# Optimization experiments

Measured on AMD Instinct MI355X. Metric: run time of the kernel, lower is better.

The kernel has to match this reference:

```python
import jax, jax.numpy as jnp
import numpy as np

HEADS = 16
EPS = 1e-5

def _ln(t):
    # LayerNorm over last axis, no affine params
    mu = jnp.mean(t, axis=-1, keepdims=True)
    var = jnp.var(t, axis=-1, keepdims=True)
    return (t - mu) / jnp.sqrt(var + EPS)

def setup_inputs() -> dict:
    key = jax.random.key(0)
    ks = jax.random.split(key, 8)
    b, n, dim, mlp_dim = 4, 2048, 1024, 4096
    s = lambda d: 1.0 / np.sqrt(d)
    return {
        "x": jax.random.normal(ks[0], (b, n, dim), dtype=jnp.float32),
        "Wqkv": jax.random.uniform(ks[1], (dim, 3 * dim), jnp.float32, -s(dim), s(dim)),
        "W1": jax.random.uniform(ks[2], (dim, mlp_dim), jnp.float32, -s(dim), s(dim)),
        "b1": jax.random.uniform(ks[3], (mlp_dim,), jnp.float32, -s(dim), s(dim)),
        "W2": jax.random.uniform(ks[4], (mlp_dim, dim), jnp.float32, -s(mlp_dim), s(mlp_dim)),
        "b2": jax.random.uniform(ks[5], (dim,), jnp.float32, -s(mlp_dim), s(mlp_dim)),
        "Wout": jax.random.uniform(ks[6], (dim, dim), jnp.float32, -s(dim), s(dim)),
        "bout": jax.random.uniform(ks[7], (dim,), jnp.float32, -s(dim), s(dim)),
    }

def reference(x, Wqkv, W1, b1, W2, b2, Wout, bout):
    b, n, dim = x.shape
    h = HEADS
    d = dim // h
    scale = dim ** (-0.5)  # NOTE: module scales by full dim, not head_dim
    qkv = x @ Wqkv  # [b, n, 3*dim]
    qkv = qkv.reshape(b, n, 3, h, d).transpose(2, 0, 3, 1, 4)  # [3, b, h, n, d]
    q, k, v = qkv[0], qkv[1], qkv[2]
    q, k = _ln(q), _ln(k)
    dots = jnp.einsum('bhid,bhjd->bhij', q, k) * scale
    attn = jax.nn.softmax(dots, axis=-1)
    attn_v = jnp.einsum('bhij,bhjd->bhid', attn, v)
    attn_v = attn_v.transpose(0, 2, 1, 3).reshape(b, n, dim)
    attn_out = attn_v @ Wout + bout
    parallel = jax.nn.gelu(x @ W1 + b1, approximate=False) @ W2 + b2
    return _ln(attn_out + parallel)
```

## Files before the change

### kernel.cpp

```cpp
#include <hip/hip_runtime.h>

typedef __attribute__((ext_vector_type(8))) short s16x8;
typedef __attribute__((ext_vector_type(4))) short s16x4;
typedef __attribute__((ext_vector_type(4))) float f32x4;
typedef __attribute__((ext_vector_type(16))) float f32x16;
typedef __attribute__((ext_vector_type(2))) unsigned uint2v;

#define DEVINL __device__ __forceinline__

DEVINL float b2f(short u){ return __uint_as_float(((unsigned)(unsigned short)u) << 16); }
DEVINL short f2bf(float f){
  unsigned u = __float_as_uint(f);
  u += 0x7fffu + ((u >> 16) & 1u);
  return (short)(u >> 16);
}
DEVINL unsigned cvtpk(float lo, float hi){
  unsigned r;
  asm("v_cvt_pk_bf16_f32 %0, %1, %2" : "=v"(r) : "v"(lo), "v"(hi));
  return r;
}
DEVINL float max3f(float a, float b, float c){
  float r; asm("v_max3_f32 %0, %1, %2, %3" : "=v"(r) : "v"(a), "v"(b), "v"(c)); return r;
}

#if __has_builtin(__builtin_amdgcn_exp2f)
#define EXP2F __builtin_amdgcn_exp2f
#else
#define EXP2F exp2f
#endif

DEVINL f32x4 mfma32(s16x8 a, s16x8 b, f32x4 c){
  return __builtin_amdgcn_mfma_f32_16x16x32_bf16(a, b, c, 0, 0, 0);
}
DEVINL f32x16 mfma3216(s16x8 a, s16x8 b, f32x16 c){
  return __builtin_amdgcn_mfma_f32_32x32x16_bf16(a, b, c, 0, 0, 0);
}

DEVINL uint2v pl32swap(unsigned a, unsigned b){
#if __has_builtin(__builtin_amdgcn_permlane32_swap)
  return __builtin_amdgcn_permlane32_swap(a, b, false, false);
#else
  asm volatile("v_permlane32_swap_b32 %0, %1" : "+v"(a), "+v"(b));
  uint2v r; r[0] = a; r[1] = b; return r;
#endif
}

typedef const unsigned __attribute__((address_space(1)))* gas1;
typedef unsigned __attribute__((address_space(3)))* las3;
DEVINL void gload16(const short* g, short* l){
  __builtin_amdgcn_global_load_lds((gas1)g, (las3)l, 16, 0, 0);
}

#define CFENCE asm volatile("" ::: "memory")
#define PBAR  do{ CFENCE; __builtin_amdgcn_sched_barrier(0); __builtin_amdgcn_s_barrier(); \
                  __builtin_amdgcn_sched_barrier(0); CFENCE; }while(0)
#define VMW8 asm volatile("s_waitcnt vmcnt(8)" ::: "memory")
#define VMW4 asm volatile("s_waitcnt vmcnt(4)" ::: "memory")
#define VMW0 asm volatile("s_waitcnt vmcnt(0)" ::: "memory")
#define PRIO1 __builtin_amdgcn_s_setprio(1)
#define PRIO0 __builtin_amdgcn_s_setprio(0)

static const int Bc   = 4;
static const int Nc   = 2048;
static const int DIM  = 1024;
static const int Tc   = Bc * Nc;
static const int MLP  = 4096;
static const int D3   = 3072;

static const size_t OFF_XB    = 0;
static const size_t OFF_WQKVT = OFF_XB    + 16777216;
static const size_t OFF_W1T   = OFF_WQKVT + 6291456;
static const size_t OFF_W2T   = OFF_W1T   + 8388608;
static const size_t OFF_WOUTT = OFF_W2T   + 8388608;
static const size_t OFF_QKV   = OFF_WOUTT + 2097152;
static const size_t OFF_QLN   = OFF_QKV   + 50331648;
static const size_t OFF_KLN   = OFF_QLN   + 16777216;
static const size_t OFF_VT    = OFF_KLN   + 16777216;
static const size_t OFF_ATTNV = OFF_VT    + 16777216;
static const size_t OFF_H     = OFF_QKV;
static const size_t OFF_S2    = OFF_KLN;

__global__ __launch_bounds__(256) void conv_x(const float* __restrict__ x, short* __restrict__ xb){
  size_t i = ((size_t)blockIdx.x * 256 + threadIdx.x) * 8;
  f32x4 v0 = *(const f32x4*)(x + i);
  f32x4 v1 = *(const f32x4*)(x + i + 4);
  s16x8 o;
#pragma unroll
  for (int j = 0; j < 4; ++j){ o[j] = f2bf(v0[j]); o[4+j] = f2bf(v1[j]); }
  *(s16x8*)(xb + i) = o;
}

__global__ __launch_bounds__(256) void transpose_conv(const float* __restrict__ W, short* __restrict__ Wt,
                                                      int K, int N){
  __shared__ float tile[32][33];
  int ntx = N >> 5;
  int tx = blockIdx.x % ntx, ty = blockIdx.x / ntx;
  int r = threadIdx.x >> 3, c = (threadIdx.x & 7) * 4;
  f32x4 v = *(const f32x4*)(W + (size_t)(ty*32 + r)*N + tx*32 + c);
  tile[r][c] = v[0]; tile[r][c+1] = v[1]; tile[r][c+2] = v[2]; tile[r][c+3] = v[3];
  __syncthreads();
  s16x4 o;
#pragma unroll
  for (int j = 0; j < 4; ++j) o[j] = f2bf(tile[c+j][r]);
  *(s16x4*)(Wt + (size_t)(tx*32 + r)*K + ty*32 + c) = o;
}

template<int ACT, int FUSED>
__global__ __launch_bounds__(256, 2) void gemmCF(const short* __restrict__ A, const short* __restrict__ A2,
                                                 const short* __restrict__ Bt, const short* __restrict__ Bt2,
                                                 short* __restrict__ C,
                                                 const float* __restrict__ bias, const float* __restrict__ bias2,
                                                 int M, int N, int K1, int K2){
  __shared__ short lds[32768];

  const int tid = threadIdx.x;
  const int w = tid >> 6, lane = tid & 63;
  const int lr = lane & 15, g = lane >> 4;
  const int wr = w >> 1, wc = w & 1;
  const int NT1 = K1 >> 6;
  const int NT = NT1 + (FUSED ? (K2 >> 6) : 0);
  const int NIT = NT >> 1;

  const int nbn = N >> 7;
  const int cpx = gridDim.x >> 3;
  const int bid = (int)blockIdx.x;
  const int sw = (bid & 7)*cpx + (bid >> 3);
  const int nbn8 = nbn >> 3;
  const int T8 = sw >> 6, t64 = sw & 63;
  const int bm = (T8 / nbn8)*8 + (t64 >> 3);
  const int bn = (T8 % nbn8)*8 + (t64 & 7);

  const int l2 = lane >> 2;
  const int gsw = ((lane & 3) - ((lane >> 3) & 3)) & 3;
  const int cof = gsw * 8;
  const int qsw8 = ((g + (lr >> 1)) & 3) * 8;

  const short* ap0h = A  + (size_t)(bm*128 + w*16 + l2)*K1 + cof;
  const short* bp0h = Bt + (size_t)(bn*128 + w*16 + l2)*K1 + cof;
  const short* ap0a = FUSED ? (A2  + (size_t)(bm*128 + w*16 + l2)*K2 + cof) : nullptr;
  const short* bp0a = FUSED ? (Bt2 + (size_t)(bn*128 + w*16 + l2)*K2 + cof) : nullptr;

  auto stA = [&](int s, int T_, int kk){
    short* d0 = lds + s*4096 + w*512;
    if (FUSED && T_ >= NT1){
      size_t off = (size_t)(T_ - NT1)*64 + kk*32;
      gload16(ap0a + off, d0);
      gload16(ap0a + (size_t)64*K2 + off, d0 + 2048);
    } else {
      size_t off = (size_t)T_*64 + kk*32;
      gload16(ap0h + off, d0);
      gload16(ap0h + (size_t)64*K1 + off, d0 + 2048);
    }
  };
  auto stB = [&](int s, int T_, int kk){
    short* d0 = lds + 16384 + s*4096 + w*512;
    if (FUSED && T_ >= NT1){
      size_t off = (size_t)(T_ - NT1)*64 + kk*32;
      gload16(bp0a + off, d0);
      gload16(bp0a + (size_t)64*K2 + off, d0 + 2048);
    } else {
      size_t off = (size_t)T_*64 + kk*32;
      gload16(bp0h + off, d0);
      gload16(bp0h + (size_t)64*K1 + off, d0 + 2048);
    }
  };

#define LDA(s, mi) (*(const s16x8*)&lds[(s)*4096 + (wr*64 + (mi)*16 + lr)*32 + qsw8])
#define LDB(s, ni) (*(const s16x8*)&lds[16384 + (s)*4096 + (wc*64 + (ni)*16 + lr)*32 + qsw8])

  f32x4 acc[4][4] = {};
#define MM(ai, r) \
  acc[r][0]=mfma32(ai,b0,acc[r][0]); acc[r][1]=mfma32(ai,b1,acc[r][1]); \
  acc[r][2]=mfma32(ai,b2,acc[r][2]); acc[r][3]=mfma32(ai,b3,acc[r][3]);
#define RD(s) s16x8 a0=LDA(s,0),a1=LDA(s,1),a2=LDA(s,2),a3=LDA(s,3), \
                    b0=LDB(s,0),b1=LDB(s,1),b2=LDB(s,2),b3=LDB(s,3);
#define MM16 MM(a0,0) MM(a1,1) MM(a2,2) MM(a3,3)

  stA(0,0,0); stB(0,0,0);
  stA(1,0,1); stB(1,0,1);
  stA(2,1,0); stB(2,1,0);
  VMW8;
  PBAR;

  for (int i = 0; i < NIT; ++i){
    const int t = i << 1;
    const bool more = (i + 1 < NIT);
    {
      RD(0)
      stA(3, t+1, 1); stB(3, t+1, 1);
      PBAR; PRIO1; MM16 PRIO0;
      VMW8;
      PBAR;
    }
    {
      RD(1)
      if (more){ stA(0, t+2, 0); stB(0, t+2, 0); }
      PBAR; PRIO1; MM16 PRIO0;
      if (more){ VMW8; } else { VMW4; }
      PBAR;
    }
    {
      RD(2)
      if (more){ stA(1, t+2, 1); stB(1, t+2, 1); }
      PBAR; PRIO1; MM16 PRIO0;
      if (more){ VMW8; } else { VMW0; }
      PBAR;
    }
    {
      RD(3)
      if (more){ stA(2, t+3, 0); stB(2, t+3, 0); }
      PBAR; PRIO1; MM16 PRIO0;
      if (more){ VMW8; }
      PBAR;
    }
  }
#undef MM
#undef RD
#undef MM16
#undef LDA
#undef LDB

#pragma unroll
  for (int a = 0; a < 4; ++a){
#pragma unroll
    for (int ni = 0; ni < 4; ++ni){
      const int col = wc*64 + ni*16 + lr;
      float bv = bias ? bias[bn*128 + col] : 0.f;
      if (FUSED && bias2) bv += bias2[bn*128 + col];
      f32x4 v = acc[a][ni];
#pragma unroll
      for (int ii = 0; ii < 4; ++ii){
        float val = v[ii] + bv;
        if constexpr (ACT) val = 0.5f*val*(1.f + erff(val*0.70710678118f));
        lds[(wr*64 + a*16 + 4*g + ii)*128 + col] = f2bf(val);
      }
    }
  }
  __syncthreads();
  const size_t crow0 = (size_t)bm * 128;
  const int ch = (tid & 15) * 8;
#pragma unroll
  for (int p = 0; p < 8; ++p){
    const int row = p*16 + (tid >> 4);
    *(s16x8*)&C[(crow0 + row)*N + bn*128 + ch] = *(const s16x8*)&lds[row*128 + ch];
  }
}

__global__ __launch_bounds__(256) void ln_reorg(const short* __restrict__ qkv, short* __restrict__ qln,
                                                short* __restrict__ kln, short* __restrict__ vtb){
  __shared__ short vtile[64*72];
  int bh = blockIdx.x >> 5, tch = blockIdx.x & 31;
  int b = bh >> 4, h = bh & 15;
  int tq = threadIdx.x >> 2, j = threadIdx.x & 3;
  size_t row = (size_t)b*Nc + tch*64 + tq;
  const short* base = qkv + row*D3 + h*64 + j*16;
  size_t orow = ((size_t)bh*Nc + tch*64 + tq)*64 + j*16;

#pragma unroll
  for (int part = 0; part < 2; ++part){
    const short* src = base + part*DIM;
    s16x8 u0 = *(const s16x8*)src;
    s16x8 u1 = *(const s16x8*)(src + 8);
    float f[16]; float s = 0.f, sq = 0.f;
#pragma unroll
    for (int i = 0; i < 8; ++i){ f[i] = b2f(u0[i]); f[8+i] = b2f(u1[i]); }
#pragma unroll
    for (int i = 0; i < 16; ++i){ s += f[i]; sq += f[i]*f[i]; }
    s  += __shfl_xor(s, 1);  s  += __shfl_xor(s, 2);
    sq += __shfl_xor(sq, 1); sq += __shfl_xor(sq, 2);
    float mu = s * (1.f/64.f);
    float var = sq * (1.f/64.f) - mu*mu;
    float inv = rsqrtf(var + 1e-5f) * (part == 0 ? 0.04508422003f : 1.f);
    s16x8 o0, o1;
#pragma unroll
    for (int i = 0; i < 8; ++i){ o0[i] = f2bf((f[i]-mu)*inv); o1[i] = f2bf((f[8+i]-mu)*inv); }
    short* dst = (part == 0 ? qln : kln) + orow;
    *(s16x8*)dst = o0; *(s16x8*)(dst + 8) = o1;
  }

  s16x8 v0 = *(const s16x8*)(base + 2*DIM);
  s16x8 v1 = *(const s16x8*)(base + 2*DIM + 8);
  *(s16x8*)&vtile[tq*72 + j*16]     = v0;
  *(s16x8*)&vtile[tq*72 + j*16 + 8] = v1;
  __syncthreads();
  s16x8 o0, o1;
#pragma unroll
  for (int i = 0; i < 8; ++i){
    o0[i] = vtile[(j*16 + i)*72 + tq];
    o1[i] = vtile[(j*16 + 8 + i)*72 + tq];
  }
  short* vdst = vtb + ((size_t)bh*64 + tq)*Nc + tch*64 + j*16;
  *(s16x8*)vdst = o0; *(s16x8*)(vdst + 8) = o1;
}

__global__ __launch_bounds__(256) void attn_kern(const short* __restrict__ qln, const short* __restrict__ kln,
                                                 const short* __restrict__ vtb, short* __restrict__ attnv){
  __shared__ short Ks[2][64*72];
  __shared__ short Vs[2][64*72];
  const int tid = threadIdx.x;
  const int bh = blockIdx.x >> 4, qt = blockIdx.x & 15;
  const int b = bh >> 4, h = bh & 15;
  const int w = tid >> 6, lane = tid & 63;
  const int lq = lane & 31, hi = lane >> 5;
  const int qrow = qt*128 + w*32 + lq;

  const short* qp = qln + ((size_t)bh*Nc + qrow)*64 + hi*8;
  s16x8 qf[4];
#pragma unroll
  for (int m = 0; m < 4; ++m) qf[m] = *(const s16x8*)(qp + m*16);

  f32x16 o0 = {0,0,0,0,0,0,0,0,0,0,0,0,0,0,0,0};
  f32x16 o1 = {0,0,0,0,0,0,0,0,0,0,0,0,0,0,0,0};
  float mrun = -INFINITY, l = 0.f;

  const int sr = tid >> 3;
  const int sc = (tid & 7) * 8;
  const short* kb0 = kln + (size_t)bh*Nc*64;
  const short* vb0 = vtb + (size_t)bh*64*Nc;

  s16x8 kr0, kr1, vr0, vr1;
  {
    kr0 = *(const s16x8*)(kb0 + (size_t)sr*64 + sc);
    kr1 = *(const s16x8*)(kb0 + (size_t)(32 + sr)*64 + sc);
    vr0 = *(const s16x8*)(vb0 + (size_t)sr*Nc + sc);
    vr1 = *(const s16x8*)(vb0 + (size_t)(32 + sr)*Nc + sc);
  }

  for (int kt = 0; kt < 32; ++kt){
    const int cur = kt & 1;
    *(s16x8*)&Ks[cur][sr*72 + sc]        = kr0;
    *(s16x8*)&Ks[cur][(32 + sr)*72 + sc] = kr1;
    *(s16x8*)&Vs[cur][sr*72 + sc]        = vr0;
    *(s16x8*)&Vs[cur][(32 + sr)*72 + sc] = vr1;
    __syncthreads();
    if (kt + 1 < 32){
      const short* kb = kb0 + (size_t)(kt+1)*64*64;
      const short* vb = vb0 + (kt+1)*64;
      kr0 = *(const s16x8*)(kb + (size_t)sr*64 + sc);
      kr1 = *(const s16x8*)(kb + (size_t)(32 + sr)*64 + sc);
      vr0 = *(const s16x8*)(vb + (size_t)sr*Nc + sc);
      vr1 = *(const s16x8*)(vb + (size_t)(32 + sr)*Nc + sc);
    }

    f32x16 st0 = {0,0,0,0,0,0,0,0,0,0,0,0,0,0,0,0};
    f32x16 st1 = {0,0,0,0,0,0,0,0,0,0,0,0,0,0,0,0};
#pragma unroll
    for (int m = 0; m < 4; ++m){
      s16x8 kf0 = *(const s16x8*)&Ks[cur][ lq      *72 + m*16 + hi*8];
      s16x8 kf1 = *(const s16x8*)&Ks[cur][(32 + lq)*72 + m*16 + hi*8];
      st0 = mfma3216(kf0, qf[m], st0);
      st1 = mfma3216(kf1, qf[m], st1);
    }

    float cmax = max3f(st0[0], st0[1], st0[2]);
    cmax = max3f(cmax, st0[3], st0[4]);   cmax = max3f(cmax, st0[5], st0[6]);
    cmax = max3f(cmax, st0[7], st0[8]);   cmax = max3f(cmax, st0[9], st0[10]);
    cmax = max3f(cmax, st0[11], st0[12]); cmax = max3f(cmax, st0[13], st0[14]);
    cmax = max3f(cmax, st0[15], st1[0]);  cmax = max3f(cmax, st1[1], st1[2]);
    cmax = max3f(cmax, st1[3], st1[4]);   cmax = max3f(cmax, st1[5], st1[6]);
    cmax = max3f(cmax, st1[7], st1[8]);   cmax = max3f(cmax, st1[9], st1[10]);
    cmax = max3f(cmax, st1[11], st1[12]); cmax = max3f(cmax, st1[13], st1[14]);
    cmax = fmaxf(cmax, st1[15]);
    cmax = fmaxf(cmax, __shfl_xor(cmax, 32));
    if (__any(cmax > mrun + 8.f)){
      float mnew = fmaxf(mrun, cmax);
      float fr = EXP2F(mrun - mnew);
      l *= fr;
#pragma unroll
      for (int r = 0; r < 16; ++r){ o0[r] *= fr; o1[r] *= fr; }
      mrun = mnew;
    }
    float p0[16], p1[16];
#pragma unroll
    for (int r = 0; r < 16; ++r){
      p0[r] = EXP2F(st0[r] - mrun); l += p0[r];
      p1[r] = EXP2F(st1[r] - mrun); l += p1[r];
    }

#pragma unroll
    for (int kc = 0; kc < 2; ++kc){
      const float* p = kc ? p1 : p0;
#pragma unroll
      for (int kh = 0; kh < 2; ++kh){
        int r0 = kh*8;
        unsigned wa = cvtpk(p[r0+0], p[r0+1]);
        unsigned wb = cvtpk(p[r0+4], p[r0+5]);
        unsigned wc2 = cvtpk(p[r0+2], p[r0+3]);
        unsigned wd = cvtpk(p[r0+6], p[r0+7]);
        uint2v s1 = pl32swap(wa, wb);
        uint2v s2 = pl32swap(wc2, wd);
        union { unsigned u[4]; s16x8 v; } pu;
        pu.u[0] = s1[0]; pu.u[1] = s2[0]; pu.u[2] = s1[1]; pu.u[3] = s2[1];
        s16x8 vf0 = *(const s16x8*)&Vs[cur][ lq      *72 + kc*32 + kh*16 + hi*8];
        s16x8 vf1 = *(const s16x8*)&Vs[cur][(32 + lq)*72 + kc*32 + kh*16 + hi*8];
        o0 = mfma3216(vf0, pu.v, o0);
        o1 = mfma3216(vf1, pu.v, o1);
      }
    }
  }

  l += __shfl_xor(l, 32);
  float inv = 1.f / l;
  short* orow = attnv + ((size_t)(b*Nc + qrow))*DIM + h*64;
#pragma unroll
  for (int r = 0; r < 16; r += 2){
    int dv = (r&3) + 8*(r>>2) + 4*hi;
    *(unsigned*)&orow[dv]      = cvtpk(o0[r]*inv, o0[r+1]*inv);
    *(unsigned*)&orow[32 + dv] = cvtpk(o1[r]*inv, o1[r+1]*inv);
  }
}

__global__ __launch_bounds__(256) void final_ln(const short* __restrict__ s2, float* __restrict__ out){
  __shared__ float red[16];
  int row = blockIdx.x, tid = threadIdx.x;
  size_t base = (size_t)row*DIM + tid*4;
  s16x4 a = *(const s16x4*)(s2 + base);
  float v[4]; float s = 0.f, sq = 0.f;
#pragma unroll
  for (int i = 0; i < 4; ++i){ v[i] = b2f(a[i]); s += v[i]; sq += v[i]*v[i]; }
#pragma unroll
  for (int m = 1; m < 64; m <<= 1){ s += __shfl_xor(s, m); sq += __shfl_xor(sq, m); }
  int wv = tid >> 6;
  if ((tid & 63) == 0){ red[wv] = s; red[8 + wv] = sq; }
  __syncthreads();
  if (tid == 0){
    float S = red[0] + red[1] + red[2] + red[3];
    float Q = red[8] + red[9] + red[10] + red[11];
    float mu = S * (1.f/1024.f);
    float var = Q * (1.f/1024.f) - mu*mu;
    red[12] = mu; red[13] = rsqrtf(var + 1e-5f);
  }
  __syncthreads();
  float mu = red[12], inv = red[13];
#pragma unroll
  for (int i = 0; i < 4; ++i) out[base + i] = (v[i] - mu) * inv;
}

extern "C" void kernel_launch(void* const* d_in, const int* in_sizes, int n_in,
                              void* d_out, int out_size, void* d_ws, size_t ws_size,
                              hipStream_t stream){
  const float* x    = (const float*)d_in[0];
  const float* Wqkv = (const float*)d_in[1];
  const float* W1   = (const float*)d_in[2];
  const float* b1   = (const float*)d_in[3];
  const float* W2   = (const float*)d_in[4];
  const float* b2   = (const float*)d_in[5];
  const float* Wout = (const float*)d_in[6];
  const float* bout = (const float*)d_in[7];
  float* out = (float*)d_out;
  char* ws = (char*)d_ws;

  short* xb    = (short*)(ws + OFF_XB);
  short* wqkvt = (short*)(ws + OFF_WQKVT);
  short* w1t   = (short*)(ws + OFF_W1T);
  short* w2t   = (short*)(ws + OFF_W2T);
  short* woutt = (short*)(ws + OFF_WOUTT);
  short* qkv   = (short*)(ws + OFF_QKV);
  short* qln   = (short*)(ws + OFF_QLN);
  short* kln   = (short*)(ws + OFF_KLN);
  short* vtb   = (short*)(ws + OFF_VT);
  short* attnv = (short*)(ws + OFF_ATTNV);
  short* hbuf  = (short*)(ws + OFF_H);
  short* s2    = (short*)(ws + OFF_S2);

  conv_x<<<4096, 256, 0, stream>>>(x, xb);
  transpose_conv<<<(DIM/32)*(D3/32),  256, 0, stream>>>(Wqkv, wqkvt, DIM, D3);
  transpose_conv<<<(DIM/32)*(MLP/32), 256, 0, stream>>>(W1, w1t, DIM, MLP);
  transpose_conv<<<(MLP/32)*(DIM/32), 256, 0, stream>>>(W2, w2t, MLP, DIM);
  transpose_conv<<<(DIM/32)*(DIM/32), 256, 0, stream>>>(Wout, woutt, DIM, DIM);

  gemmCF<0,0><<<(Tc/128)*(D3/128), 256, 0, stream>>>(xb, xb, wqkvt, wqkvt, qkv,
                                                     nullptr, nullptr, Tc, D3, DIM, DIM);
  ln_reorg<<<64*32, 256, 0, stream>>>(qkv, qln, kln, vtb);
  attn_kern<<<64*16, 256, 0, stream>>>(qln, kln, vtb, attnv);

  gemmCF<1,0><<<(Tc/128)*(MLP/128), 256, 0, stream>>>(xb, xb, w1t, w1t, hbuf,
                                                      b1, nullptr, Tc, MLP, DIM, DIM);
  gemmCF<0,1><<<(Tc/128)*(DIM/128), 256, 0, stream>>>(hbuf, attnv, w2t, woutt, s2,
                                                      b2, bout, Tc, DIM, MLP, DIM);

  final_ln<<<Tc, 256, 0, stream>>>(s2, out);
}
```

Measured before the change: 419.2 us.

## Add 256x256-tile 8-wave GEMM kernel for QKV and W1 projections

Adds a new GEMM kernel with 256x256 output tiles, 512 threads (8 waves) and 128KB LDS double buffering, split into four quarter-phases. Each phase interleaves async global-to-LDS loads of the next tile with MFMA work, using barriers and raised wave priority. It also adds an XCD-aware block swizzle. The QKV and W1 projections use it in place of the 128x128 kernel, aiming for higher arithmetic intensity and less global traffic per FLOP. The cost is fewer blocks (384 and 512), which risks tail imbalance and lower occupancy. The frequent barriers may also stall waves.

```diff
diff --git a/kernel.cpp b/kernel.cpp
--- a/kernel.cpp
+++ b/kernel.cpp
@@ -54,6 +54,9 @@
 #define CFENCE asm volatile("" ::: "memory")
 #define PBAR  do{ CFENCE; __builtin_amdgcn_sched_barrier(0); __builtin_amdgcn_s_barrier(); \
                   __builtin_amdgcn_sched_barrier(0); CFENCE; }while(0)
+#define RBAR  __builtin_amdgcn_s_barrier()
+#define LGKM0 do{ asm volatile("s_waitcnt lgkmcnt(0)" ::: "memory"); \
+                  __builtin_amdgcn_sched_barrier(0); }while(0)
 #define VMW8 asm volatile("s_waitcnt vmcnt(8)" ::: "memory")
 #define VMW4 asm volatile("s_waitcnt vmcnt(4)" ::: "memory")
 #define VMW0 asm volatile("s_waitcnt vmcnt(0)" ::: "memory")
@@ -103,6 +106,155 @@
 #pragma unroll
   for (int j = 0; j < 4; ++j) o[j] = f2bf(tile[c+j][r]);
   *(s16x4*)(Wt + (size_t)(tx*32 + r)*K + ty*32 + c) = o;
+}
+
+template<int ACT>
+__global__ __launch_bounds__(512, 2) void gemm8q(const short* __restrict__ A, const short* __restrict__ Bt,
+                                                 short* __restrict__ C, const float* __restrict__ bias,
+                                                 int M, int N, int K){
+  __shared__ short lds[65536];
+  short* Ab = lds;
+  short* Bb = lds + 32768;
+
+  const int tid = threadIdx.x;
+  const int w = tid >> 6, lane = tid & 63;
+  const int lr = lane & 15, g = lane >> 4;
+  const int wr = w >> 2, wc = w & 3;
+  const int NT = K >> 6;
+
+  const int nbn = N >> 8;
+  const int cpx = gridDim.x >> 3;
+  const int bid = (int)blockIdx.x;
+  const int sw = (bid & 7)*cpx + (bid >> 3);
+  const int bm = sw / nbn, bn = sw % nbn;
+
+  const int l2 = lane >> 2;
+  const int gsw = ((lane & 3) - ((lane >> 3) & 3)) & 3;
+  const int cof = gsw * 8;
+  const int qsw8 = ((g + (lr >> 1)) & 3) * 8;
+
+  const short* ap0 = A  + (size_t)(bm*256 + w*16 + l2)*K + cof;
+  const short* bp0 = Bt + (size_t)(bn*256 + w*16 + l2)*K + cof;
+
+#define STA2(buf, T_, kk) do{ \
+    gload16(ap0 + (size_t)(T_)*64 + (kk)*32,                   Ab + (((buf)*2+(kk))*2+0)*4096 + w*512); \
+    gload16(ap0 + (size_t)128*K + (size_t)(T_)*64 + (kk)*32,   Ab + (((buf)*2+(kk))*2+1)*4096 + w*512); }while(0)
+#define STB2(buf, T_, kk) do{ \
+    gload16(bp0 + (size_t)(T_)*64 + (kk)*32,                   Bb + ((buf)*2+(kk))*8192 + w*512); \
+    gload16(bp0 + (size_t)128*K + (size_t)(T_)*64 + (kk)*32,   Bb + ((buf)*2+(kk))*8192 + 4096 + w*512); }while(0)
+#define LA(buf, kk, mi) (*(const s16x8*)&Ab[(((buf)*2+(kk))*2+wr)*4096 + ((mi)*16 + lr)*32 + qsw8])
+#define LB(buf, kk, ni) (*(const s16x8*)&Bb[((buf)*2+(kk))*8192 + (wc*64 + (ni)*16 + lr)*32 + qsw8])
+
+  f32x4 acc[8][4] = {};
+
+  STA2(0,0,0); STB2(0,0,0);
+  STA2(0,0,1); STB2(0,0,1);
+  VMW0;
+  RBAR;
+
+  for (int t = 0; t < NT; ++t){
+    const int buf = t & 1, nb = buf ^ 1;
+    const bool more = (t + 1 < NT);
+
+    {
+      s16x8 af[8];
+#pragma unroll
+      for (int mi = 0; mi < 8; ++mi) af[mi] = LA(buf, 0, mi);
+      s16x8 b0 = LB(buf, 0, 0), b1 = LB(buf, 0, 1);
+      if (more) STA2(nb, t+1, 0);
+      RBAR;
+      LGKM0;
+      PRIO1;
+#pragma unroll
+      for (int mi = 0; mi < 8; ++mi){
+        acc[mi][0] = mfma32(af[mi], b0, acc[mi][0]);
+        acc[mi][1] = mfma32(af[mi], b1, acc[mi][1]);
+      }
+      PRIO0;
+      RBAR;
+    }
+    {
+      s16x8 af[8];
+#pragma unroll
+      for (int mi = 0; mi < 8; ++mi) af[mi] = LA(buf, 0, mi);
+      s16x8 b0 = LB(buf, 0, 2), b1 = LB(buf, 0, 3);
+      if (more) STB2(nb, t+1, 0);
+      RBAR;
+      LGKM0;
+      PRIO1;
+#pragma unroll
+      for (int mi = 0; mi < 8; ++mi){
+        acc[mi][2] = mfma32(af[mi], b0, acc[mi][2]);
+        acc[mi][3] = mfma32(af[mi], b1, acc[mi][3]);
+      }
+      PRIO0;
+      if (more){ VMW4; } else { VMW0; }
+      RBAR;
+    }
+    {
+      s16x8 af[8];
+#pragma unroll
+      for (int mi = 0; mi < 8; ++mi) af[mi] = LA(buf, 1, mi);
+      s16x8 b0 = LB(buf, 1, 0), b1 = LB(buf, 1, 1);
+      if (more) STA2(nb, t+1, 1);
+      RBAR;
+      LGKM0;
+      PRIO1;
+#pragma unroll
+      for (int mi = 0; mi < 8; ++mi){
+        acc[mi][0] = mfma32(af[mi], b0, acc[mi][0]);
+        acc[mi][1] = mfma32(af[mi], b1, acc[mi][1]);
+      }
+      PRIO0;
+      RBAR;
+    }
+    {
+      s16x8 af[8];
+#pragma unroll
+      for (int mi = 0; mi < 8; ++mi) af[mi] = LA(buf, 1, mi);
+      s16x8 b0 = LB(buf, 1, 2), b1 = LB(buf, 1, 3);
+      if (more) STB2(nb, t+1, 1);
+      RBAR;
+      LGKM0;
+      PRIO1;
+#pragma unroll
+      for (int mi = 0; mi < 8; ++mi){
+        acc[mi][2] = mfma32(af[mi], b0, acc[mi][2]);
+        acc[mi][3] = mfma32(af[mi], b1, acc[mi][3]);
+      }
+      PRIO0;
+      if (more){ VMW4; }
+      RBAR;
+    }
+  }
+#undef STA2
+#undef STB2
+#undef LA
+#undef LB
+
+#pragma unroll
+  for (int mi = 0; mi < 8; ++mi){
+#pragma unroll
+    for (int ni = 0; ni < 4; ++ni){
+      const int col = wc*64 + ni*16 + lr;
+      const float bv = bias ? bias[bn*256 + col] : 0.f;
+      f32x4 v = acc[mi][ni];
+#pragma unroll
+      for (int ii = 0; ii < 4; ++ii){
+        float val = v[ii] + bv;
+        if constexpr (ACT) val = 0.5f*val*(1.f + erff(val*0.70710678118f));
+        lds[(wr*128 + mi*16 + 4*g + ii)*256 + col] = f2bf(val);
+      }
+    }
+  }
+  __syncthreads();
+  const size_t crow0 = (size_t)bm * 256;
+  const int ch = (tid & 31) * 8;
+#pragma unroll
+  for (int p = 0; p < 16; ++p){
+    const int row = p*16 + (tid >> 5);
+    *(s16x8*)&C[(crow0 + row)*N + bn*256 + ch] = *(const s16x8*)&lds[row*256 + ch];
+  }
 }
 
 template<int ACT, int FUSED>
@@ -469,13 +621,11 @@
   transpose_conv<<<(MLP/32)*(DIM/32), 256, 0, stream>>>(W2, w2t, MLP, DIM);
   transpose_conv<<<(DIM/32)*(DIM/32), 256, 0, stream>>>(Wout, woutt, DIM, DIM);
 
-  gemmCF<0,0><<<(Tc/128)*(D3/128), 256, 0, stream>>>(xb, xb, wqkvt, wqkvt, qkv,
-                                                     nullptr, nullptr, Tc, D3, DIM, DIM);
+  gemm8q<0><<<(Tc/256)*(D3/256), 512, 0, stream>>>(xb, wqkvt, qkv, nullptr, Tc, D3, DIM);
   ln_reorg<<<64*32, 256, 0, stream>>>(qkv, qln, kln, vtb);
   attn_kern<<<64*16, 256, 0, stream>>>(qln, kln, vtb, attnv);
 
-  gemmCF<1,0><<<(Tc/128)*(MLP/128), 256, 0, stream>>>(xb, xb, w1t, w1t, hbuf,
-                                                      b1, nullptr, Tc, MLP, DIM, DIM);
+  gemm8q<1><<<(Tc/256)*(MLP/256), 512, 0, stream>>>(xb, w1t, hbuf, b1, Tc, MLP, DIM);
   gemmCF<0,1><<<(Tc/128)*(DIM/128), 256, 0, stream>>>(hbuf, attnv, w2t, woutt, s2,
                                                       b2, bout, Tc, DIM, MLP, DIM);
 
```

New measurement: 439.0 us. +4.7%, slower.

## Add larger-tile 512-thread GEMM for QKV and MLP-up projections

Applied to the files above, without the earlier changes.

Introduces a new GEMM kernel with 8 waves per block and 128x256 or 256x256 output tiles, a K-step of 32, double-buffered direct-to-LDS loads, swizzled LDS reads, and a block-index swizzle meant to improve L2 locality. It replaces the 128x128 kernel for the QKV projection and for the GELU MLP-up projection. The larger tiles raise arithmetic intensity and cut global reloads of A and B. The trade-offs are higher register pressure, fewer blocks for the smaller QKV grid, and an epilogue staged through LDS in chunks.

```diff
diff --git a/kernel.cpp b/kernel.cpp
--- a/kernel.cpp
+++ b/kernel.cpp
@@ -103,6 +103,139 @@
 #pragma unroll
   for (int j = 0; j < 4; ++j) o[j] = f2bf(tile[c+j][r]);
   *(s16x4*)(Wt + (size_t)(tx*32 + r)*K + ty*32 + c) = o;
+}
+
+template<int BM, int ACT>
+__global__ __launch_bounds__(512, 2) void gemmSX(const short* __restrict__ A, const short* __restrict__ Bt,
+                                                 short* __restrict__ C, const float* __restrict__ bias,
+                                                 int M, int N, int K){
+  constexpr int MREP = BM/32;
+  constexpr int ABUF = BM*32;
+  constexpr int LDSN = (BM==256) ? 32768 : 24576;
+  __shared__ short lds[LDSN];
+  short* Ab = lds;
+  short* Bb = lds + 2*ABUF;
+
+  const int tid = threadIdx.x;
+  const int w = tid >> 6, lane = tid & 63;
+  const int lr = lane & 15, g = lane >> 4;
+  const int wr = w >> 2, wc = w & 3;
+  const int NT = K >> 5;
+
+  const int nbn = N >> 8;
+  const int cpx = gridDim.x >> 3;
+  const int bid = (int)blockIdx.x;
+  const int sw = (bid & 7)*cpx + (bid >> 3);
+  const int bm = sw / nbn, bn = sw % nbn;
+
+  const int gsw = ((tid & 3) - ((tid >> 3) & 3)) & 3;
+  const int qsw8 = ((g + (lr >> 1)) & 3) * 8;
+
+  const size_t aK128 = (size_t)128 * K;
+  const short* agA = A  + (size_t)(bm*BM  + (tid >> 2))*K + gsw*8;
+  const short* agB = Bt + (size_t)(bn*256 + (tid >> 2))*K + gsw*8;
+
+  auto STAGE = [&](int bf, int T){
+    const size_t ko = (size_t)T * 32;
+    if constexpr (BM == 256){
+      gload16(agA + ko,          Ab + bf*ABUF + w*512);
+      gload16(agA + ko + aK128,  Ab + bf*ABUF + 4096 + w*512);
+    } else {
+      gload16(agA + ko,          Ab + bf*ABUF + w*512);
+    }
+    gload16(agB + ko,          Bb + bf*8192 + w*512);
+    gload16(agB + ko + aK128,  Bb + bf*8192 + 4096 + w*512);
+  };
+
+  f32x4 acc[MREP][4] = {};
+
+  STAGE(0, 0);
+  __syncthreads();
+
+  for (int t = 0; t < NT; ++t){
+    const int buf = t & 1;
+    if (t + 1 < NT) STAGE(buf ^ 1, t + 1);
+
+    s16x8 af[MREP];
+#pragma unroll
+    for (int mi = 0; mi < MREP; ++mi)
+      af[mi] = *(const s16x8*)&Ab[buf*ABUF + (wr*(BM/2) + mi*16 + lr)*32 + qsw8];
+    s16x8 b0 = *(const s16x8*)&Bb[buf*8192 + (wc*64 +  0 + lr)*32 + qsw8];
+    s16x8 b1 = *(const s16x8*)&Bb[buf*8192 + (wc*64 + 16 + lr)*32 + qsw8];
+    s16x8 b2 = *(const s16x8*)&Bb[buf*8192 + (wc*64 + 32 + lr)*32 + qsw8];
+    s16x8 b3 = *(const s16x8*)&Bb[buf*8192 + (wc*64 + 48 + lr)*32 + qsw8];
+#pragma unroll
+    for (int mi = 0; mi < MREP; ++mi){
+      acc[mi][0] = mfma32(af[mi], b0, acc[mi][0]);
+      acc[mi][1] = mfma32(af[mi], b1, acc[mi][1]);
+      acc[mi][2] = mfma32(af[mi], b2, acc[mi][2]);
+      acc[mi][3] = mfma32(af[mi], b3, acc[mi][3]);
+    }
+    __syncthreads();
+  }
+
+  if constexpr (BM == 256){
+#pragma unroll
+    for (int h = 0; h < 2; ++h){
+      if (wr == h){
+#pragma unroll
+        for (int mi = 0; mi < 8; ++mi){
+#pragma unroll
+          for (int ni = 0; ni < 4; ++ni){
+            const int col = wc*64 + ni*16 + lr;
+            const float bv = bias ? bias[bn*256 + col] : 0.f;
+            f32x4 v = acc[mi][ni];
+#pragma unroll
+            for (int ii = 0; ii < 4; ++ii){
+              float val = v[ii] + bv;
+              if constexpr (ACT) val = 0.5f*val*(1.f + erff(val*0.70710678118f));
+              lds[(mi*16 + 4*g + ii)*256 + col] = f2bf(val);
+            }
+          }
+        }
+      }
+      __syncthreads();
+      const int ch = (tid & 31) * 8;
+#pragma unroll
+      for (int p = 0; p < 8; ++p){
+        const int row = p*16 + (tid >> 5);
+        *(s16x8*)&C[(size_t)(bm*256 + h*128 + row)*N + bn*256 + ch] =
+            *(const s16x8*)&lds[row*256 + ch];
+      }
+      __syncthreads();
+    }
+  } else {
+#pragma unroll
+    for (int q = 0; q < 4; ++q){
+      if (wr == (q >> 1)){
+#pragma unroll
+        for (int m2 = 0; m2 < 2; ++m2){
+          const int mi = (q & 1)*2 + m2;
+#pragma unroll
+          for (int ni = 0; ni < 4; ++ni){
+            const int col = wc*64 + ni*16 + lr;
+            const float bv = bias ? bias[bn*256 + col] : 0.f;
+            f32x4 v = acc[mi][ni];
+#pragma unroll
+            for (int ii = 0; ii < 4; ++ii){
+              float val = v[ii] + bv;
+              if constexpr (ACT) val = 0.5f*val*(1.f + erff(val*0.70710678118f));
+              lds[(m2*16 + 4*g + ii)*256 + col] = f2bf(val);
+            }
+          }
+        }
+      }
+      __syncthreads();
+      const int ch = (tid & 31) * 8;
+#pragma unroll
+      for (int p = 0; p < 2; ++p){
+        const int row = p*16 + (tid >> 5);
+        *(s16x8*)&C[(size_t)(bm*128 + q*32 + row)*N + bn*256 + ch] =
+            *(const s16x8*)&lds[row*256 + ch];
+      }
+      __syncthreads();
+    }
+  }
 }
 
 template<int ACT, int FUSED>
@@ -469,13 +602,11 @@
   transpose_conv<<<(MLP/32)*(DIM/32), 256, 0, stream>>>(W2, w2t, MLP, DIM);
   transpose_conv<<<(DIM/32)*(DIM/32), 256, 0, stream>>>(Wout, woutt, DIM, DIM);
 
-  gemmCF<0,0><<<(Tc/128)*(D3/128), 256, 0, stream>>>(xb, xb, wqkvt, wqkvt, qkv,
-                                                     nullptr, nullptr, Tc, D3, DIM, DIM);
+  gemmSX<128,0><<<(Tc/128)*(D3/256), 512, 0, stream>>>(xb, wqkvt, qkv, nullptr, Tc, D3, DIM);
   ln_reorg<<<64*32, 256, 0, stream>>>(qkv, qln, kln, vtb);
   attn_kern<<<64*16, 256, 0, stream>>>(qln, kln, vtb, attnv);
 
-  gemmCF<1,0><<<(Tc/128)*(MLP/128), 256, 0, stream>>>(xb, xb, w1t, w1t, hbuf,
-                                                      b1, nullptr, Tc, MLP, DIM, DIM);
+  gemmSX<256,1><<<(Tc/256)*(MLP/256), 512, 0, stream>>>(xb, w1t, hbuf, b1, Tc, MLP, DIM);
   gemmCF<0,1><<<(Tc/128)*(DIM/128), 256, 0, stream>>>(hbuf, attnv, w2t, woutt, s2,
                                                       b2, bout, Tc, DIM, MLP, DIM);
 
```

Result: slower. 451.0 us (+7.6%).

## Fuse per-head Q/K LayerNorm and V transpose into QKV GEMM epilogue

Applied to the files above, without the earlier changes.

The QKV projection GEMM now normalizes Q and K per head and writes them, along with transposed V, directly in the attention layout from its shared-memory tile. The separate ln_reorg kernel and the intermediate qkv buffer are removed. This avoids a full write and reread of the qkv tensor plus one kernel launch. The cost is a heavier GEMM epilogue with a padded LDS stride and strided transpose reads, and the LayerNorm statistics are now computed on bf16-rounded values as before.

```diff
diff --git a/kernel.cpp b/kernel.cpp
--- a/kernel.cpp
+++ b/kernel.cpp
@@ -105,12 +105,14 @@
   *(s16x4*)(Wt + (size_t)(tx*32 + r)*K + ty*32 + c) = o;
 }
 
-template<int ACT, int FUSED>
+template<int ACT, int FUSED, int QKVEPI>
 __global__ __launch_bounds__(256, 2) void gemmCF(const short* __restrict__ A, const short* __restrict__ A2,
                                                  const short* __restrict__ Bt, const short* __restrict__ Bt2,
                                                  short* __restrict__ C,
                                                  const float* __restrict__ bias, const float* __restrict__ bias2,
-                                                 int M, int N, int K1, int K2){
+                                                 int M, int N, int K1, int K2,
+                                                 short* __restrict__ qln, short* __restrict__ kln,
+                                                 short* __restrict__ vtb){
   __shared__ short lds[32768];
 
   const int tid = threadIdx.x;
@@ -220,6 +222,66 @@
 #undef LDA
 #undef LDB
 
+  if constexpr (QKVEPI){
+#pragma unroll
+    for (int a = 0; a < 4; ++a){
+#pragma unroll
+      for (int ni = 0; ni < 4; ++ni){
+        const int col = wc*64 + ni*16 + lr;
+        f32x4 v = acc[a][ni];
+#pragma unroll
+        for (int ii = 0; ii < 4; ++ii)
+          lds[(wr*64 + a*16 + 4*g + ii)*130 + col] = f2bf(v[ii]);
+      }
+    }
+    __syncthreads();
+    const int part = (bn*128) >> 10;
+    const int h0 = ((bn*128) & 1023) >> 6;
+    const int rg = bm*128;
+    const int b = rg >> 11;
+    const int tok0 = rg & 2047;
+
+    if (part < 2){
+      short* dstbase = part ? kln : qln;
+      const float sc = part ? 1.f : 0.04508422003f;
+      const int row = tid >> 1, grp = tid & 1;
+      const short* src = &lds[row*130 + grp*64];
+      float s = 0.f, sq = 0.f;
+#pragma unroll
+      for (int i2 = 0; i2 < 8; ++i2){
+        s16x8 u = *(const s16x8*)(src + i2*8);
+#pragma unroll
+        for (int j = 0; j < 8; ++j){ float fv = b2f(u[j]); s += fv; sq += fv*fv; }
+      }
+      const float mu = s * (1.f/64.f);
+      const float var = sq * (1.f/64.f) - mu*mu;
+      const float inv = rsqrtf(var + 1e-5f) * sc;
+      const int bh = b*16 + h0 + grp;
+      short* dst = dstbase + ((size_t)bh*Nc + tok0 + row)*64;
+#pragma unroll
+      for (int i2 = 0; i2 < 8; ++i2){
+        s16x8 u = *(const s16x8*)(src + i2*8);
+        s16x8 o;
+#pragma unroll
+        for (int j = 0; j < 8; ++j) o[j] = f2bf((b2f(u[j]) - mu) * inv);
+        *(s16x8*)(dst + i2*8) = o;
+      }
+    } else {
+      const int d = tid & 63, hh = (tid >> 6) & 1, half = tid >> 7;
+      const int bh = b*16 + h0 + hh;
+      short* dst = vtb + ((size_t)bh*64 + d)*Nc + tok0 + half*64;
+#pragma unroll
+      for (int i2 = 0; i2 < 8; ++i2){
+        s16x8 o;
+#pragma unroll
+        for (int j = 0; j < 8; ++j)
+          o[j] = lds[(half*64 + i2*8 + j)*130 + hh*64 + d];
+        *(s16x8*)(dst + i2*8) = o;
+      }
+    }
+    return;
+  }
+
 #pragma unroll
   for (int a = 0; a < 4; ++a){
 #pragma unroll
@@ -244,53 +306,6 @@
     const int row = p*16 + (tid >> 4);
     *(s16x8*)&C[(crow0 + row)*N + bn*128 + ch] = *(const s16x8*)&lds[row*128 + ch];
   }
-}
-
-__global__ __launch_bounds__(256) void ln_reorg(const short* __restrict__ qkv, short* __restrict__ qln,
-                                                short* __restrict__ kln, short* __restrict__ vtb){
-  __shared__ short vtile[64*72];
-  int bh = blockIdx.x >> 5, tch = blockIdx.x & 31;
-  int b = bh >> 4, h = bh & 15;
-  int tq = threadIdx.x >> 2, j = threadIdx.x & 3;
-  size_t row = (size_t)b*Nc + tch*64 + tq;
-  const short* base = qkv + row*D3 + h*64 + j*16;
-  size_t orow = ((size_t)bh*Nc + tch*64 + tq)*64 + j*16;
-
-#pragma unroll
-  for (int part = 0; part < 2; ++part){
-    const short* src = base + part*DIM;
-    s16x8 u0 = *(const s16x8*)src;
-    s16x8 u1 = *(const s16x8*)(src + 8);
-    float f[16]; float s = 0.f, sq = 0.f;
-#pragma unroll
-    for (int i = 0; i < 8; ++i){ f[i] = b2f(u0[i]); f[8+i] = b2f(u1[i]); }
-#pragma unroll
-    for (int i = 0; i < 16; ++i){ s += f[i]; sq += f[i]*f[i]; }
-    s  += __shfl_xor(s, 1);  s  += __shfl_xor(s, 2);
-    sq += __shfl_xor(sq, 1); sq += __shfl_xor(sq, 2);
-    float mu = s * (1.f/64.f);
-    float var = sq * (1.f/64.f) - mu*mu;
-    float inv = rsqrtf(var + 1e-5f) * (part == 0 ? 0.04508422003f : 1.f);
-    s16x8 o0, o1;
-#pragma unroll
-    for (int i = 0; i < 8; ++i){ o0[i] = f2bf((f[i]-mu)*inv); o1[i] = f2bf((f[8+i]-mu)*inv); }
-    short* dst = (part == 0 ? qln : kln) + orow;
-    *(s16x8*)dst = o0; *(s16x8*)(dst + 8) = o1;
-  }
-
-  s16x8 v0 = *(const s16x8*)(base + 2*DIM);
-  s16x8 v1 = *(const s16x8*)(base + 2*DIM + 8);
-  *(s16x8*)&vtile[tq*72 + j*16]     = v0;
-  *(s16x8*)&vtile[tq*72 + j*16 + 8] = v1;
-  __syncthreads();
-  s16x8 o0, o1;
-#pragma unroll
-  for (int i = 0; i < 8; ++i){
-    o0[i] = vtile[(j*16 + i)*72 + tq];
-    o1[i] = vtile[(j*16 + 8 + i)*72 + tq];
-  }
-  short* vdst = vtb + ((size_t)bh*64 + tq)*Nc + tch*64 + j*16;
-  *(s16x8*)vdst = o0; *(s16x8*)(vdst + 8) = o1;
 }
 
 __global__ __launch_bounds__(256) void attn_kern(const short* __restrict__ qln, const short* __restrict__ kln,
@@ -455,7 +470,6 @@
   short* w1t   = (short*)(ws + OFF_W1T);
   short* w2t   = (short*)(ws + OFF_W2T);
   short* woutt = (short*)(ws + OFF_WOUTT);
-  short* qkv   = (short*)(ws + OFF_QKV);
   short* qln   = (short*)(ws + OFF_QLN);
   short* kln   = (short*)(ws + OFF_KLN);
   short* vtb   = (short*)(ws + OFF_VT);
@@ -469,15 +483,17 @@
   transpose_conv<<<(MLP/32)*(DIM/32), 256, 0, stream>>>(W2, w2t, MLP, DIM);
   transpose_conv<<<(DIM/32)*(DIM/32), 256, 0, stream>>>(Wout, woutt, DIM, DIM);
 
-  gemmCF<0,0><<<(Tc/128)*(D3/128), 256, 0, stream>>>(xb, xb, wqkvt, wqkvt, qkv,
-                                                     nullptr, nullptr, Tc, D3, DIM, DIM);
-  ln_reorg<<<64*32, 256, 0, stream>>>(qkv, qln, kln, vtb);
+  gemmCF<0,0,1><<<(Tc/128)*(D3/128), 256, 0, stream>>>(xb, xb, wqkvt, wqkvt, nullptr,
+                                                       nullptr, nullptr, Tc, D3, DIM, DIM,
+                                                       qln, kln, vtb);
   attn_kern<<<64*16, 256, 0, stream>>>(qln, kln, vtb, attnv);
 
-  gemmCF<1,0><<<(Tc/128)*(MLP/128), 256, 0, stream>>>(xb, xb, w1t, w1t, hbuf,
-                                                      b1, nullptr, Tc, MLP, DIM, DIM);
-  gemmCF<0,1><<<(Tc/128)*(DIM/128), 256, 0, stream>>>(hbuf, attnv, w2t, woutt, s2,
-                                                      b2, bout, Tc, DIM, MLP, DIM);
+  gemmCF<1,0,0><<<(Tc/128)*(MLP/128), 256, 0, stream>>>(xb, xb, w1t, w1t, hbuf,
+                                                        b1, nullptr, Tc, MLP, DIM, DIM,
+                                                        nullptr, nullptr, nullptr);
+  gemmCF<0,1,0><<<(Tc/128)*(DIM/128), 256, 0, stream>>>(hbuf, attnv, w2t, woutt, s2,
+                                                        b2, bout, Tc, DIM, MLP, DIM,
+                                                        nullptr, nullptr, nullptr);
 
   final_ln<<<Tc, 256, 0, stream>>>(s2, out);
 }
```

Measured after the change: 414.1 us (median of 2 runs). About the same (-1.2%).
